# Optimization experiments

Hardware: AMD Instinct MI355X
Metric: run time of the kernel (lower is better)

Reference implementation:

```python
import jax, jax.numpy as jnp
import numpy as np

B, S, E = 16, 1024, 512
D = 2 * E            # dim of concatenated embeddings, input to QKV and MLP
H1, H2 = 2048, 1024  # hidden_dims
SCALE = float(1.0 / np.sqrt(E))  # code scales by embedding_dim**0.5 (the init arg, not D)


def setup_inputs() -> dict:
    key = jax.random.key(0)
    k = jax.random.split(key, 12)

    def lin_w(kk, fan_in, fan_out):
        return jax.random.normal(kk, (fan_in, fan_out), jnp.float32) * float(1.0 / np.sqrt(fan_in))

    return {
        "emb1": jax.random.normal(k[0], (B, S, E), jnp.float32),
        "emb2": jax.random.normal(k[1], (B, S, E), jnp.float32),
        # query-row masks; all ones (a 0 would -inf an entire softmax row -> NaN)
        "mask1": jnp.ones((B, S // 2), jnp.int32),
        "mask2": jnp.ones((B, S // 2), jnp.int32),
        "Wq": lin_w(k[2], D, D), "bq": jnp.zeros((D,), jnp.float32),
        "Wk": lin_w(k[3], D, D), "bk": jnp.zeros((D,), jnp.float32),
        "Wv": lin_w(k[4], D, D), "bv": jnp.zeros((D,), jnp.float32),
        "W1": lin_w(k[5], D, H1), "b1": jnp.zeros((H1,), jnp.float32),
        "W2": lin_w(k[6], H1, H2), "b2": jnp.zeros((H2,), jnp.float32),
        "W3": lin_w(k[7], H2, 1), "b3": jnp.zeros((1,), jnp.float32),
    }


def reference(emb1, emb2, mask1, mask2, Wq, bq, Wk, bk, Wv, bv, W1, b1, W2, b2, W3, b3):
    x = jnp.concatenate([emb1, emb2], axis=-1)        # [B, S, D]
    mask = jnp.concatenate([mask1, mask2], axis=-1)   # [B, S] (query-row mask)

    # QKV self-attention with query-only mask
    Q = x @ Wq + bq
    K = x @ Wk + bk
    V = x @ Wv + bv
    scores = jnp.einsum("bqd,bkd->bqk", Q, K) * SCALE  # [B, S, S]
    scores = jnp.where(mask[:, :, None] == 0, -jnp.inf, scores)
    attn = jax.nn.softmax(scores, axis=-1)
    attended = jnp.einsum("bqk,bkd->bqd", attn, V)     # [B, S, D]

    # MLP head (Dropout is identity in eval mode)
    h = jax.nn.relu(attended @ W1 + b1)
    h = jax.nn.relu(h @ W2 + b2)
    logits = h @ W3 + b3                               # [B, S, 1]
    return jax.nn.sigmoid(logits)
```

## Files before the change

### kernel.cpp

```cpp
#include <hip/hip_runtime.h>
#include <math.h>

#define DEV __device__ __forceinline__

typedef unsigned short u16;
typedef unsigned int   u32;
typedef __bf16 bf16x8 __attribute__((ext_vector_type(8)));
typedef float  f32x4  __attribute__((ext_vector_type(4)));
typedef u16    u16x8  __attribute__((ext_vector_type(8)));
typedef u16    u16x4  __attribute__((ext_vector_type(4)));

DEV u16 f2b(float f) {
  u32 u = __builtin_bit_cast(u32, f);
  u = (u + 0x7FFFu + ((u >> 16) & 1u)) >> 16;
  return (u16)u;
}
DEV float b2f(u16 h) { u32 u = (u32)h << 16; return __builtin_bit_cast(float, u); }

DEV void gl_lds16(const u16* g, u16* l) {
  __builtin_amdgcn_global_load_lds((const __attribute__((address_space(1))) void*)g,
                                   (__attribute__((address_space(3))) void*)l, 16, 0, 0);
}

DEV float wred_max(float v) {
#pragma unroll
  for (int o = 32; o > 0; o >>= 1) v = fmaxf(v, __shfl_xor(v, o, 64));
  return v;
}
DEV float wred_sum(float v) {
#pragma unroll
  for (int o = 32; o > 0; o >>= 1) v += __shfl_xor(v, o, 64);
  return v;
}

__global__ __launch_bounds__(256) void concat_convert(
    const float* __restrict__ e1, const float* __restrict__ e2, u16* __restrict__ xb) {
  const size_t idx = ((size_t)blockIdx.x * 256 + threadIdx.x) * 8;
  const int d = (int)(idx & 1023);
  const size_t row = idx >> 10;
  const float* s = (d < 512) ? (e1 + row * 512 + d) : (e2 + row * 512 + (d - 512));
  f32x4 a = *(const f32x4*)s;
  f32x4 b = *(const f32x4*)(s + 4);
  u16x8 o;
  o[0]=f2b(a[0]); o[1]=f2b(a[1]); o[2]=f2b(a[2]); o[3]=f2b(a[3]);
  o[4]=f2b(b[0]); o[5]=f2b(b[1]); o[6]=f2b(b[2]); o[7]=f2b(b[3]);
  *(u16x8*)(xb + idx) = o;
}

__global__ __launch_bounds__(256) void transpose_w(
    const float* __restrict__ W, int ldi, u16* __restrict__ WT, int ldo) {
  __shared__ float tile[64][65];
  const int tx = threadIdx.x & 63, ty = threadIdx.x >> 6;
  const int r0 = blockIdx.y * 64, c0 = blockIdx.x * 64;
#pragma unroll
  for (int i = 0; i < 16; ++i)
    tile[ty + 4*i][tx] = W[(size_t)(r0 + ty + 4*i) * ldi + c0 + tx];
  __syncthreads();
#pragma unroll
  for (int i = 0; i < 16; ++i)
    WT[(size_t)(c0 + ty + 4*i) * ldo + r0 + tx] = f2b(tile[tx][ty + 4*i]);
}

__global__ void concat_bias(const float* __restrict__ bq, const float* __restrict__ bk,
                            float* __restrict__ o) {
  int i = blockIdx.x * 256 + threadIdx.x;
  o[i] = (i < 1024) ? bq[i] : bk[i - 1024];
}

template<int F32OUT, int RELU, int RBIAS>
__global__ __launch_bounds__(512, 2) void gemm256(
    const u16* __restrict__ A, int lda, long long sA,
    const u16* __restrict__ B, int ldb, long long sB,
    void* __restrict__ C, int ldc, long long sC,
    const float* __restrict__ bias, float scale, int K) {
  __shared__ __align__(16) u16 lds[4][2][8192];

  const int t  = threadIdx.x;
  const int ln = t & 63, wv = t >> 6;

  int bx, by, bz;
  {
    const int gx = gridDim.x, gy = gridDim.y, gz = gridDim.z;
    const int nwg = gx * gy * gz;
    const int F = (blockIdx.z * gy + blockIdx.y) * gx + blockIdx.x;
    const int q = nwg >> 3;
    const int L = (F & 7) * q + (F >> 3);
    if (gz > 1) {
      const int pb = gx * gy;
      bz = L / pb; const int r = L - bz * pb;
      by = r / gx; bx = r - by * gx;
    } else {
      bz = 0;
      const int sh = ((gy & 7) == 0) ? 8 : 4;
      const int sw = gx * sh;
      const int sy = L / sw; const int r = L - sy * sw;
      bx = r / sh; by = sy * sh + (r - bx * sh);
    }
  }
  const int m0 = by * 256, n0 = bx * 256;
  A += (size_t)bz * (size_t)sA; B += (size_t)bz * (size_t)sB;

  const int srow = t >> 2;
  const int sgr  = (t & 3) ^ ((t >> 3) & 3);
  const u16* gA = A + (size_t)(m0 + srow) * lda + sgr * 8;
  const u16* gB = B + (size_t)(n0 + srow) * ldb + sgr * 8;
  const size_t a128 = (size_t)128 * lda, b128 = (size_t)128 * ldb;
  const int ldst = wv * 512;

  const int l15 = ln & 15, lhi = ln >> 4;
  const int wm = (wv >> 2) * 128, wn = (wv & 3) * 64;

  int offA[8], offB[4];
#pragma unroll
  for (int i = 0; i < 8; ++i) {
    const int r = wm + i * 16 + l15;
    offA[i] = r * 32 + ((lhi ^ ((r >> 1) & 3)) << 3);
  }
#pragma unroll
  for (int j = 0; j < 4; ++j) {
    const int r = wn + j * 16 + l15;
    offB[j] = r * 32 + ((lhi ^ ((r >> 1) & 3)) << 3);
  }

  f32x4 acc[8][4] = {};
  const int KT = K >> 5;

#pragma unroll
  for (int pt = 0; pt < 3; ++pt) {
    const u16* _ga = gA + (size_t)pt * 32;
    const u16* _gb = gB + (size_t)pt * 32;
    u16* _la = &lds[pt][0][ldst];
    u16* _lb = &lds[pt][1][ldst];
    gl_lds16(_ga, _la); gl_lds16(_ga + a128, _la + 4096);
    gl_lds16(_gb, _lb); gl_lds16(_gb + b128, _lb + 4096);
  }
  asm volatile("s_waitcnt vmcnt(8)" ::: "memory");
  __builtin_amdgcn_sched_barrier(0);
  __builtin_amdgcn_s_barrier();

  for (int kt = 0; kt < KT; ++kt) {
    const u16* Abuf = &lds[kt & 3][0][0];
    const u16* Bbuf = &lds[kt & 3][1][0];
    const int  nt   = kt + 3;

    if (nt < KT) {
      const u16* _ga = gA + (size_t)nt * 32;
      const u16* _gb = gB + (size_t)nt * 32;
      u16* _la = &lds[nt & 3][0][ldst];
      u16* _lb = &lds[nt & 3][1][ldst];
      gl_lds16(_ga, _la); gl_lds16(_ga + a128, _la + 4096);
      gl_lds16(_gb, _lb); gl_lds16(_gb + b128, _lb + 4096);
    }

    bf16x8 a0 = *(const bf16x8*)&Abuf[offA[0]];
    bf16x8 a1 = *(const bf16x8*)&Abuf[offA[1]];
    bf16x8 a2 = *(const bf16x8*)&Abuf[offA[2]];
    bf16x8 a3 = *(const bf16x8*)&Abuf[offA[3]];
    bf16x8 b0 = *(const bf16x8*)&Bbuf[offB[0]];
    bf16x8 b1 = *(const bf16x8*)&Bbuf[offB[1]];
    bf16x8 b2 = *(const bf16x8*)&Bbuf[offB[2]];
    bf16x8 b3 = *(const bf16x8*)&Bbuf[offB[3]];
    bf16x8 a4 = *(const bf16x8*)&Abuf[offA[4]];
    bf16x8 a5 = *(const bf16x8*)&Abuf[offA[5]];
    bf16x8 a6 = *(const bf16x8*)&Abuf[offA[6]];
    bf16x8 a7 = *(const bf16x8*)&Abuf[offA[7]];

    __builtin_amdgcn_s_setprio(1);
    acc[0][0] = __builtin_amdgcn_mfma_f32_16x16x32_bf16(a0, b0, acc[0][0], 0, 0, 0);
    acc[0][1] = __builtin_amdgcn_mfma_f32_16x16x32_bf16(a0, b1, acc[0][1], 0, 0, 0);
    acc[0][2] = __builtin_amdgcn_mfma_f32_16x16x32_bf16(a0, b2, acc[0][2], 0, 0, 0);
    acc[0][3] = __builtin_amdgcn_mfma_f32_16x16x32_bf16(a0, b3, acc[0][3], 0, 0, 0);
    acc[1][0] = __builtin_amdgcn_mfma_f32_16x16x32_bf16(a1, b0, acc[1][0], 0, 0, 0);
    acc[1][1] = __builtin_amdgcn_mfma_f32_16x16x32_bf16(a1, b1, acc[1][1], 0, 0, 0);
    acc[1][2] = __builtin_amdgcn_mfma_f32_16x16x32_bf16(a1, b2, acc[1][2], 0, 0, 0);
    acc[1][3] = __builtin_amdgcn_mfma_f32_16x16x32_bf16(a1, b3, acc[1][3], 0, 0, 0);
    acc[2][0] = __builtin_amdgcn_mfma_f32_16x16x32_bf16(a2, b0, acc[2][0], 0, 0, 0);
    acc[2][1] = __builtin_amdgcn_mfma_f32_16x16x32_bf16(a2, b1, acc[2][1], 0, 0, 0);
    acc[2][2] = __builtin_amdgcn_mfma_f32_16x16x32_bf16(a2, b2, acc[2][2], 0, 0, 0);
    acc[2][3] = __builtin_amdgcn_mfma_f32_16x16x32_bf16(a2, b3, acc[2][3], 0, 0, 0);
    acc[3][0] = __builtin_amdgcn_mfma_f32_16x16x32_bf16(a3, b0, acc[3][0], 0, 0, 0);
    acc[3][1] = __builtin_amdgcn_mfma_f32_16x16x32_bf16(a3, b1, acc[3][1], 0, 0, 0);
    acc[3][2] = __builtin_amdgcn_mfma_f32_16x16x32_bf16(a3, b2, acc[3][2], 0, 0, 0);
    acc[3][3] = __builtin_amdgcn_mfma_f32_16x16x32_bf16(a3, b3, acc[3][3], 0, 0, 0);
    acc[4][0] = __builtin_amdgcn_mfma_f32_16x16x32_bf16(a4, b0, acc[4][0], 0, 0, 0);
    acc[4][1] = __builtin_amdgcn_mfma_f32_16x16x32_bf16(a4, b1, acc[4][1], 0, 0, 0);
    acc[4][2] = __builtin_amdgcn_mfma_f32_16x16x32_bf16(a4, b2, acc[4][2], 0, 0, 0);
    acc[4][3] = __builtin_amdgcn_mfma_f32_16x16x32_bf16(a4, b3, acc[4][3], 0, 0, 0);
    acc[5][0] = __builtin_amdgcn_mfma_f32_16x16x32_bf16(a5, b0, acc[5][0], 0, 0, 0);
    acc[5][1] = __builtin_amdgcn_mfma_f32_16x16x32_bf16(a5, b1, acc[5][1], 0, 0, 0);
    acc[5][2] = __builtin_amdgcn_mfma_f32_16x16x32_bf16(a5, b2, acc[5][2], 0, 0, 0);
    acc[5][3] = __builtin_amdgcn_mfma_f32_16x16x32_bf16(a5, b3, acc[5][3], 0, 0, 0);
    acc[6][0] = __builtin_amdgcn_mfma_f32_16x16x32_bf16(a6, b0, acc[6][0], 0, 0, 0);
    acc[6][1] = __builtin_amdgcn_mfma_f32_16x16x32_bf16(a6, b1, acc[6][1], 0, 0, 0);
    acc[6][2] = __builtin_amdgcn_mfma_f32_16x16x32_bf16(a6, b2, acc[6][2], 0, 0, 0);
    acc[6][3] = __builtin_amdgcn_mfma_f32_16x16x32_bf16(a6, b3, acc[6][3], 0, 0, 0);
    acc[7][0] = __builtin_amdgcn_mfma_f32_16x16x32_bf16(a7, b0, acc[7][0], 0, 0, 0);
    acc[7][1] = __builtin_amdgcn_mfma_f32_16x16x32_bf16(a7, b1, acc[7][1], 0, 0, 0);
    acc[7][2] = __builtin_amdgcn_mfma_f32_16x16x32_bf16(a7, b2, acc[7][2], 0, 0, 0);
    acc[7][3] = __builtin_amdgcn_mfma_f32_16x16x32_bf16(a7, b3, acc[7][3], 0, 0, 0);
    __builtin_amdgcn_s_setprio(0);

    if (kt < KT - 3)       { asm volatile("s_waitcnt vmcnt(8)" ::: "memory"); }
    else if (kt == KT - 3) { asm volatile("s_waitcnt vmcnt(4)" ::: "memory"); }
    else if (kt == KT - 2) { asm volatile("s_waitcnt vmcnt(0)" ::: "memory"); }
    __builtin_amdgcn_sched_barrier(0);
    __builtin_amdgcn_s_barrier();
  }

  const size_t cb = (size_t)bz * (size_t)sC;
#pragma unroll
  for (int i = 0; i < 8; ++i) {
    const int rg = m0 + wm + i * 16 + lhi * 4;
#pragma unroll
    for (int j = 0; j < 4; ++j) {
      const int cg = n0 + wn + j * 16 + l15;
      const float cbv = (!RBIAS && bias) ? bias[cg] : 0.f;
#pragma unroll
      for (int r = 0; r < 4; ++r) {
        float v = acc[i][j][r] * scale + (RBIAS ? bias[rg + r] : cbv);
        if (RELU) v = fmaxf(v, 0.f);
        if (F32OUT) ((float*)C)[cb + (size_t)(rg + r) * ldc + cg] = v;
        else        ((u16*)C)[cb + (size_t)(rg + r) * ldc + cg] = f2b(v);
      }
    }
  }
}

__global__ __launch_bounds__(256) void softmax_mask(
    const float* __restrict__ sc, const int* __restrict__ m1,
    const int* __restrict__ m2, u16* __restrict__ attn) {
  __shared__ float red[8];
  const int row = blockIdx.x;
  const int b = row >> 10, q = row & 1023;
  const int mk = (q < 512) ? m1[b * 512 + q] : m2[b * 512 + q - 512];
  f32x4 v = ((const f32x4*)(sc + (size_t)row * 1024))[threadIdx.x];
  if (mk == 0) { v[0] = v[1] = v[2] = v[3] = -INFINITY; }
  float mx = fmaxf(fmaxf(v[0], v[1]), fmaxf(v[2], v[3]));
  mx = wred_max(mx);
  const int ln = threadIdx.x & 63, wv = threadIdx.x >> 6;
  if (ln == 0) red[wv] = mx;
  __syncthreads();
  mx = fmaxf(fmaxf(red[0], red[1]), fmaxf(red[2], red[3]));
  float e0 = __expf(v[0] - mx), e1 = __expf(v[1] - mx);
  float e2 = __expf(v[2] - mx), e3 = __expf(v[3] - mx);
  float s = wred_sum(e0 + e1 + e2 + e3);
  if (ln == 0) red[4 + wv] = s;
  __syncthreads();
  const float inv = 1.f / (red[4] + red[5] + red[6] + red[7]);
  u16x4 o; o[0] = f2b(e0 * inv); o[1] = f2b(e1 * inv); o[2] = f2b(e2 * inv); o[3] = f2b(e3 * inv);
  *(u16x4*)(attn + (size_t)row * 1024 + threadIdx.x * 4) = o;
}

__global__ __launch_bounds__(256) void logits_sigmoid(
    const u16* __restrict__ h2, const float* __restrict__ W3,
    const float* __restrict__ b3, float* __restrict__ out) {
  const int wid = (blockIdx.x * 256 + threadIdx.x) >> 6;
  const int ln = threadIdx.x & 63;
  const u16* r = h2 + (size_t)wid * 1024 + ln * 16;
  u16x8 v0 = *(const u16x8*)r;
  u16x8 v1 = *(const u16x8*)(r + 8);
  const float* w = W3 + ln * 16;
  float s = 0.f;
#pragma unroll
  for (int i = 0; i < 8; ++i) s += b2f(v0[i]) * w[i];
#pragma unroll
  for (int i = 0; i < 8; ++i) s += b2f(v1[i]) * w[8 + i];
#pragma unroll
  for (int o = 32; o > 0; o >>= 1) s += __shfl_down(s, o, 64);
  if (ln == 0) out[wid] = 1.f / (1.f + __expf(-(s + b3[0])));
}

extern "C" void kernel_launch(void* const* d_in, const int* in_sizes, int n_in,
                              void* d_out, int out_size, void* d_ws, size_t ws_size,
                              hipStream_t stream) {
  (void)in_sizes; (void)n_in; (void)out_size; (void)ws_size;
  const float* emb1 = (const float*)d_in[0];
  const float* emb2 = (const float*)d_in[1];
  const int*   mask1 = (const int*)d_in[2];
  const int*   mask2 = (const int*)d_in[3];
  const float* Wq = (const float*)d_in[4];  const float* bq = (const float*)d_in[5];
  const float* Wk = (const float*)d_in[6];  const float* bk = (const float*)d_in[7];
  const float* Wv = (const float*)d_in[8];  const float* bv = (const float*)d_in[9];
  const float* W1 = (const float*)d_in[10]; const float* b1 = (const float*)d_in[11];
  const float* W2 = (const float*)d_in[12]; const float* b2 = (const float*)d_in[13];
  const float* W3 = (const float*)d_in[14]; const float* b3 = (const float*)d_in[15];

  char* ws = (char*)d_ws;
  u16*  XB    = (u16*)(ws + 0);
  u16*  QK    = (u16*)(ws + 33554432);
  u16*  VT    = (u16*)(ws + 100663296);
  float* SC   = (float*)(ws + 134217728);
  u16*  WTQKV = (u16*)(ws + 201326592);
  u16*  W1T   = (u16*)(ws + 207618048);
  u16*  W2T   = (u16*)(ws + 211812352);
  float* BF_  = (float*)(ws + 216006656);
  u16*  ATTN  = XB;
  u16*  ATT   = (u16*)(ws + 134217728);
  u16*  H1    = QK;
  u16*  H2    = VT;
  float* out  = (float*)d_out;

  const float SCALE = 0.04419417382415922f;

  concat_convert<<<8192, 256, 0, stream>>>(emb1, emb2, XB);
  transpose_w<<<dim3(16, 16), 256, 0, stream>>>(Wq, 1024, WTQKV, 1024);
  transpose_w<<<dim3(16, 16), 256, 0, stream>>>(Wk, 1024, WTQKV + 1024 * 1024, 1024);
  transpose_w<<<dim3(16, 16), 256, 0, stream>>>(Wv, 1024, WTQKV + 2048 * 1024, 1024);
  transpose_w<<<dim3(32, 16), 256, 0, stream>>>(W1, 2048, W1T, 1024);
  transpose_w<<<dim3(16, 32), 256, 0, stream>>>(W2, 1024, W2T, 2048);
  concat_bias<<<8, 256, 0, stream>>>(bq, bk, BF_);

  gemm256<0, 0, 0><<<dim3(8, 64, 1), 512, 0, stream>>>(
      XB, 1024, 0, WTQKV, 1024, 0, QK, 2048, 0, BF_, 1.f, 1024);
  gemm256<0, 0, 1><<<dim3(64, 4, 1), 512, 0, stream>>>(
      WTQKV + 2048 * 1024, 1024, 0, XB, 1024, 0, VT, 16384, 0, bv, 1.f, 1024);
  gemm256<1, 0, 0><<<dim3(4, 4, 16), 512, 0, stream>>>(
      QK, 2048, 2097152LL, QK + 1024, 2048, 2097152LL,
      SC, 1024, 1048576LL, nullptr, SCALE, 1024);
  softmax_mask<<<16384, 256, 0, stream>>>(SC, mask1, mask2, ATTN);
  gemm256<0, 0, 0><<<dim3(4, 4, 16), 512, 0, stream>>>(
      ATTN, 1024, 1048576LL, VT, 16384, 1024LL,
      ATT, 1024, 1048576LL, nullptr, 1.f, 1024);
  gemm256<0, 1, 0><<<dim3(8, 64, 1), 512, 0, stream>>>(
      ATT, 1024, 0, W1T, 1024, 0, H1, 2048, 0, b1, 1.f, 1024);
  gemm256<0, 1, 0><<<dim3(4, 64, 1), 512, 0, stream>>>(
      H1, 2048, 0, W2T, 2048, 0, H2, 1024, 0, b2, 1.f, 2048);
  logits_sigmoid<<<4096, 256, 0, stream>>>(H2, W3, b3, out);
}
```

Baseline: 404.0 us.

## Shrink GEMM tiles to 128x128 with 256 threads and triple-buffered LDS

```diff
diff --git a/kernel.cpp b/kernel.cpp
--- a/kernel.cpp
+++ b/kernel.cpp
@@ -68,12 +68,12 @@
 }
 
 template<int F32OUT, int RELU, int RBIAS>
-__global__ __launch_bounds__(512, 2) void gemm256(
+__global__ __launch_bounds__(256, 3) void gemm128(
     const u16* __restrict__ A, int lda, long long sA,
     const u16* __restrict__ B, int ldb, long long sB,
     void* __restrict__ C, int ldc, long long sC,
     const float* __restrict__ bias, float scale, int K) {
-  __shared__ __align__(16) u16 lds[4][2][8192];
+  __shared__ __align__(16) u16 sm[3 * 8192];
 
   const int t  = threadIdx.x;
   const int ln = t & 63, wv = t >> 6;
@@ -91,79 +91,69 @@
       by = r / gx; bx = r - by * gx;
     } else {
       bz = 0;
-      const int sh = ((gy & 7) == 0) ? 8 : 4;
-      const int sw = gx * sh;
+      const int sw = gx * 8;
       const int sy = L / sw; const int r = L - sy * sw;
-      bx = r / sh; by = sy * sh + (r - bx * sh);
+      bx = r >> 3; by = sy * 8 + (r & 7);
     }
   }
-  const int m0 = by * 256, n0 = bx * 256;
+  const int m0 = by * 128, n0 = bx * 128;
   A += (size_t)bz * (size_t)sA; B += (size_t)bz * (size_t)sB;
 
   const int srow = t >> 2;
   const int sgr  = (t & 3) ^ ((t >> 3) & 3);
   const u16* gA = A + (size_t)(m0 + srow) * lda + sgr * 8;
   const u16* gB = B + (size_t)(n0 + srow) * ldb + sgr * 8;
-  const size_t a128 = (size_t)128 * lda, b128 = (size_t)128 * ldb;
+  const size_t a64 = (size_t)64 * lda, b64 = (size_t)64 * ldb;
   const int ldst = wv * 512;
 
   const int l15 = ln & 15, lhi = ln >> 4;
-  const int wm = (wv >> 2) * 128, wn = (wv & 3) * 64;
-
-  int offA[8], offB[4];
-#pragma unroll
-  for (int i = 0; i < 8; ++i) {
+  const int wm = (wv >> 1) * 64, wn = (wv & 1) * 64;
+
+  int offA[4], offB[4];
+#pragma unroll
+  for (int i = 0; i < 4; ++i) {
     const int r = wm + i * 16 + l15;
     offA[i] = r * 32 + ((lhi ^ ((r >> 1) & 3)) << 3);
   }
 #pragma unroll
   for (int j = 0; j < 4; ++j) {
     const int r = wn + j * 16 + l15;
-    offB[j] = r * 32 + ((lhi ^ ((r >> 1) & 3)) << 3);
-  }
-
-  f32x4 acc[8][4] = {};
+    offB[j] = 4096 + r * 32 + ((lhi ^ ((r >> 1) & 3)) << 3);
+  }
+
+  f32x4 acc[4][4] = {};
   const int KT = K >> 5;
 
-#pragma unroll
-  for (int pt = 0; pt < 3; ++pt) {
-    const u16* _ga = gA + (size_t)pt * 32;
-    const u16* _gb = gB + (size_t)pt * 32;
-    u16* _la = &lds[pt][0][ldst];
-    u16* _lb = &lds[pt][1][ldst];
-    gl_lds16(_ga, _la); gl_lds16(_ga + a128, _la + 4096);
-    gl_lds16(_gb, _lb); gl_lds16(_gb + b128, _lb + 4096);
-  }
-  asm volatile("s_waitcnt vmcnt(8)" ::: "memory");
+#define STAGE(tile)                                                       \
+  {                                                                       \
+    const int rb = (tile) % 3;                                            \
+    const u16* _ga = gA + (size_t)(tile) * 32;                            \
+    const u16* _gb = gB + (size_t)(tile) * 32;                            \
+    u16* _la = &sm[rb * 8192 + ldst];                                     \
+    u16* _lb = &sm[rb * 8192 + 4096 + ldst];                              \
+    gl_lds16(_ga, _la); gl_lds16(_ga + a64, _la + 2048);                  \
+    gl_lds16(_gb, _lb); gl_lds16(_gb + b64, _lb + 2048);                  \
+  }
+
+  STAGE(0); STAGE(1);
+  asm volatile("s_waitcnt vmcnt(4)" ::: "memory");
   __builtin_amdgcn_sched_barrier(0);
   __builtin_amdgcn_s_barrier();
 
   for (int kt = 0; kt < KT; ++kt) {
-    const u16* Abuf = &lds[kt & 3][0][0];
-    const u16* Bbuf = &lds[kt & 3][1][0];
-    const int  nt   = kt + 3;
-
-    if (nt < KT) {
-      const u16* _ga = gA + (size_t)nt * 32;
-      const u16* _gb = gB + (size_t)nt * 32;
-      u16* _la = &lds[nt & 3][0][ldst];
-      u16* _lb = &lds[nt & 3][1][ldst];
-      gl_lds16(_ga, _la); gl_lds16(_ga + a128, _la + 4096);
-      gl_lds16(_gb, _lb); gl_lds16(_gb + b128, _lb + 4096);
-    }
-
-    bf16x8 a0 = *(const bf16x8*)&Abuf[offA[0]];
-    bf16x8 a1 = *(const bf16x8*)&Abuf[offA[1]];
-    bf16x8 a2 = *(const bf16x8*)&Abuf[offA[2]];
-    bf16x8 a3 = *(const bf16x8*)&Abuf[offA[3]];
-    bf16x8 b0 = *(const bf16x8*)&Bbuf[offB[0]];
-    bf16x8 b1 = *(const bf16x8*)&Bbuf[offB[1]];
-    bf16x8 b2 = *(const bf16x8*)&Bbuf[offB[2]];
-    bf16x8 b3 = *(const bf16x8*)&Bbuf[offB[3]];
-    bf16x8 a4 = *(const bf16x8*)&Abuf[offA[4]];
-    bf16x8 a5 = *(const bf16x8*)&Abuf[offA[5]];
-    bf16x8 a6 = *(const bf16x8*)&Abuf[offA[6]];
-    bf16x8 a7 = *(const bf16x8*)&Abuf[offA[7]];
+    const int rb = kt % 3;
+    const u16* Ab = &sm[rb * 8192];
+
+    if (kt + 2 < KT) STAGE(kt + 2);
+
+    bf16x8 a0 = *(const bf16x8*)&Ab[offA[0]];
+    bf16x8 a1 = *(const bf16x8*)&Ab[offA[1]];
+    bf16x8 a2 = *(const bf16x8*)&Ab[offA[2]];
+    bf16x8 a3 = *(const bf16x8*)&Ab[offA[3]];
+    bf16x8 b0 = *(const bf16x8*)&Ab[offB[0]];
+    bf16x8 b1 = *(const bf16x8*)&Ab[offB[1]];
+    bf16x8 b2 = *(const bf16x8*)&Ab[offB[2]];
+    bf16x8 b3 = *(const bf16x8*)&Ab[offB[3]];
 
     __builtin_amdgcn_s_setprio(1);
     acc[0][0] = __builtin_amdgcn_mfma_f32_16x16x32_bf16(a0, b0, acc[0][0], 0, 0, 0);
@@ -182,34 +172,20 @@
     acc[3][1] = __builtin_amdgcn_mfma_f32_16x16x32_bf16(a3, b1, acc[3][1], 0, 0, 0);
     acc[3][2] = __builtin_amdgcn_mfma_f32_16x16x32_bf16(a3, b2, acc[3][2], 0, 0, 0);
     acc[3][3] = __builtin_amdgcn_mfma_f32_16x16x32_bf16(a3, b3, acc[3][3], 0, 0, 0);
-    acc[4][0] = __builtin_amdgcn_mfma_f32_16x16x32_bf16(a4, b0, acc[4][0], 0, 0, 0);
-    acc[4][1] = __builtin_amdgcn_mfma_f32_16x16x32_bf16(a4, b1, acc[4][1], 0, 0, 0);
-    acc[4][2] = __builtin_amdgcn_mfma_f32_16x16x32_bf16(a4, b2, acc[4][2], 0, 0, 0);
-    acc[4][3] = __builtin_amdgcn_mfma_f32_16x16x32_bf16(a4, b3, acc[4][3], 0, 0, 0);
-    acc[5][0] = __builtin_amdgcn_mfma_f32_16x16x32_bf16(a5, b0, acc[5][0], 0, 0, 0);
-    acc[5][1] = __builtin_amdgcn_mfma_f32_16x16x32_bf16(a5, b1, acc[5][1], 0, 0, 0);
-    acc[5][2] = __builtin_amdgcn_mfma_f32_16x16x32_bf16(a5, b2, acc[5][2], 0, 0, 0);
-    acc[5][3] = __builtin_amdgcn_mfma_f32_16x16x32_bf16(a5, b3, acc[5][3], 0, 0, 0);
-    acc[6][0] = __builtin_amdgcn_mfma_f32_16x16x32_bf16(a6, b0, acc[6][0], 0, 0, 0);
-    acc[6][1] = __builtin_amdgcn_mfma_f32_16x16x32_bf16(a6, b1, acc[6][1], 0, 0, 0);
-    acc[6][2] = __builtin_amdgcn_mfma_f32_16x16x32_bf16(a6, b2, acc[6][2], 0, 0, 0);
-    acc[6][3] = __builtin_amdgcn_mfma_f32_16x16x32_bf16(a6, b3, acc[6][3], 0, 0, 0);
-    acc[7][0] = __builtin_amdgcn_mfma_f32_16x16x32_bf16(a7, b0, acc[7][0], 0, 0, 0);
-    acc[7][1] = __builtin_amdgcn_mfma_f32_16x16x32_bf16(a7, b1, acc[7][1], 0, 0, 0);
-    acc[7][2] = __builtin_amdgcn_mfma_f32_16x16x32_bf16(a7, b2, acc[7][2], 0, 0, 0);
-    acc[7][3] = __builtin_amdgcn_mfma_f32_16x16x32_bf16(a7, b3, acc[7][3], 0, 0, 0);
     __builtin_amdgcn_s_setprio(0);
 
-    if (kt < KT - 3)       { asm volatile("s_waitcnt vmcnt(8)" ::: "memory"); }
-    else if (kt == KT - 3) { asm volatile("s_waitcnt vmcnt(4)" ::: "memory"); }
+    if (kt < KT - 2)       { asm volatile("s_waitcnt vmcnt(4)" ::: "memory"); }
     else if (kt == KT - 2) { asm volatile("s_waitcnt vmcnt(0)" ::: "memory"); }
-    __builtin_amdgcn_sched_barrier(0);
-    __builtin_amdgcn_s_barrier();
-  }
+    if (kt < KT - 1) {
+      __builtin_amdgcn_sched_barrier(0);
+      __builtin_amdgcn_s_barrier();
+    }
+  }
+#undef STAGE
 
   const size_t cb = (size_t)bz * (size_t)sC;
 #pragma unroll
-  for (int i = 0; i < 8; ++i) {
+  for (int i = 0; i < 4; ++i) {
     const int rg = m0 + wm + i * 16 + lhi * 4;
 #pragma unroll
     for (int j = 0; j < 4; ++j) {
@@ -310,20 +286,20 @@
   transpose_w<<<dim3(16, 32), 256, 0, stream>>>(W2, 1024, W2T, 2048);
   concat_bias<<<8, 256, 0, stream>>>(bq, bk, BF_);
 
-  gemm256<0, 0, 0><<<dim3(8, 64, 1), 512, 0, stream>>>(
+  gemm128<0, 0, 0><<<dim3(16, 128, 1), 256, 0, stream>>>(
       XB, 1024, 0, WTQKV, 1024, 0, QK, 2048, 0, BF_, 1.f, 1024);
-  gemm256<0, 0, 1><<<dim3(64, 4, 1), 512, 0, stream>>>(
+  gemm128<0, 0, 1><<<dim3(128, 8, 1), 256, 0, stream>>>(
       WTQKV + 2048 * 1024, 1024, 0, XB, 1024, 0, VT, 16384, 0, bv, 1.f, 1024);
-  gemm256<1, 0, 0><<<dim3(4, 4, 16), 512, 0, stream>>>(
+  gemm128<1, 0, 0><<<dim3(8, 8, 16), 256, 0, stream>>>(
       QK, 2048, 2097152LL, QK + 1024, 2048, 2097152LL,
       SC, 1024, 1048576LL, nullptr, SCALE, 1024);
   softmax_mask<<<16384, 256, 0, stream>>>(SC, mask1, mask2, ATTN);
-  gemm256<0, 0, 0><<<dim3(4, 4, 16), 512, 0, stream>>>(
+  gemm128<0, 0, 0><<<dim3(8, 8, 16), 256, 0, stream>>>(
       ATTN, 1024, 1048576LL, VT, 16384, 1024LL,
       ATT, 1024, 1048576LL, nullptr, 1.f, 1024);
-  gemm256<0, 1, 0><<<dim3(8, 64, 1), 512, 0, stream>>>(
+  gemm128<0, 1, 0><<<dim3(16, 128, 1), 256, 0, stream>>>(
       ATT, 1024, 0, W1T, 1024, 0, H1, 2048, 0, b1, 1.f, 1024);
-  gemm256<0, 1, 0><<<dim3(4, 64, 1), 512, 0, stream>>>(
+  gemm128<0, 1, 0><<<dim3(8, 128, 1), 256, 0, stream>>>(
       H1, 2048, 0, W2T, 2048, 0, H2, 1024, 0, b2, 1.f, 2048);
   logits_sigmoid<<<4096, 256, 0, stream>>>(H2, W3, b3, out);
 }
```

New measurement: 452.5 us. 12.0% more time.

## Restructure GEMM main loop into BK=64 double-buffered ping-pong with interleaved stages

Applied to the files above, without the earlier changes.

```diff
diff --git a/kernel.cpp b/kernel.cpp
--- a/kernel.cpp
+++ b/kernel.cpp
@@ -2,6 +2,7 @@
 #include <math.h>
 
 #define DEV __device__ __forceinline__
+#define SB0() __builtin_amdgcn_sched_barrier(0)
 
 typedef unsigned short u16;
 typedef unsigned int   u32;
@@ -73,7 +74,7 @@
     const u16* __restrict__ B, int ldb, long long sB,
     void* __restrict__ C, int ldc, long long sC,
     const float* __restrict__ bias, float scale, int K) {
-  __shared__ __align__(16) u16 lds[4][2][8192];
+  __shared__ __align__(16) u16 lds[2][2][16384];
 
   const int t  = threadIdx.x;
   const int ln = t & 63, wv = t >> 6;
@@ -100,112 +101,91 @@
   const int m0 = by * 256, n0 = bx * 256;
   A += (size_t)bz * (size_t)sA; B += (size_t)bz * (size_t)sB;
 
-  const int srow = t >> 2;
-  const int sgr  = (t & 3) ^ ((t >> 3) & 3);
-  const u16* gA = A + (size_t)(m0 + srow) * lda + sgr * 8;
-  const u16* gB = B + (size_t)(n0 + srow) * ldb + sgr * 8;
-  const size_t a128 = (size_t)128 * lda, b128 = (size_t)128 * ldb;
-  const int ldst = wv * 512;
+  const int gl = (ln & 7) ^ (ln >> 3);
+  const u16* gAs = A + (size_t)(m0 + (t >> 3)) * lda + gl * 8;
+  const u16* gBs = B + (size_t)(n0 + (t >> 3)) * ldb + gl * 8;
 
   const int l15 = ln & 15, lhi = ln >> 4;
   const int wm = (wv >> 2) * 128, wn = (wv & 3) * 64;
-
-  int offA[8], offB[4];
-#pragma unroll
-  for (int i = 0; i < 8; ++i) {
-    const int r = wm + i * 16 + l15;
-    offA[i] = r * 32 + ((lhi ^ ((r >> 1) & 3)) << 3);
+  const int colk0 = ((lhi ^ (l15 & 7)) << 3);
+  const int colk1 = (((4 + lhi) ^ (l15 & 7)) << 3);
+  const int rcA = (wv >> 2) * 8192 + l15 * 64;
+  const int rcB = ((wv & 3) >> 1) * 8192 + (wv & 1) * 4096 + l15 * 64;
+
+  f32x4 acc[8][4] = {};
+  bf16x8 Af[4][2], Bf[4][2];
+  const int KT = K >> 6, NIT = KT >> 1;
+
+#define STG(T, OP, H, LD, GS)                                              \
+  if ((T) < KT) {                                                          \
+    const u16* _s = (GS) + (size_t)(H) * 128 * (size_t)(LD) + (size_t)(T) * 64; \
+    u16* _d = &lds[(T) & 1][OP][(H) * 8192 + wv * 512];                    \
+    gl_lds16(_s, _d); gl_lds16(_s + 64 * (size_t)(LD), _d + 4096);         \
   }
-#pragma unroll
-  for (int j = 0; j < 4; ++j) {
-    const int r = wn + j * 16 + l15;
-    offB[j] = r * 32 + ((lhi ^ ((r >> 1) & 3)) << 3);
+#define RDA(BUF, ILO) {                                                    \
+  _Pragma("unroll") for (int ii = 0; ii < 4; ++ii) {                       \
+    Af[ii][0] = *(const bf16x8*)&lds[BUF][0][rcA + ((ILO) + ii) * 1024 + colk0]; \
+    Af[ii][1] = *(const bf16x8*)&lds[BUF][0][rcA + ((ILO) + ii) * 1024 + colk1]; } }
+#define RDB(BUF, JLO) {                                                    \
+  _Pragma("unroll") for (int jj = 0; jj < 2; ++jj) {                       \
+    Bf[(JLO) + jj][0] = *(const bf16x8*)&lds[BUF][1][rcB + ((JLO) + jj) * 1024 + colk0]; \
+    Bf[(JLO) + jj][1] = *(const bf16x8*)&lds[BUF][1][rcB + ((JLO) + jj) * 1024 + colk1]; } }
+#define MM(ILO, JLO) {                                                     \
+  _Pragma("unroll") for (int ii = 0; ii < 4; ++ii)                         \
+  _Pragma("unroll") for (int jj = 0; jj < 2; ++jj) {                       \
+    acc[(ILO)+ii][(JLO)+jj] = __builtin_amdgcn_mfma_f32_16x16x32_bf16(Af[ii][0], Bf[(JLO)+jj][0], acc[(ILO)+ii][(JLO)+jj], 0, 0, 0); \
+    acc[(ILO)+ii][(JLO)+jj] = __builtin_amdgcn_mfma_f32_16x16x32_bf16(Af[ii][1], Bf[(JLO)+jj][1], acc[(ILO)+ii][(JLO)+jj], 0, 0, 0); } }
+#define BAR() __builtin_amdgcn_s_barrier()
+#define LGKM0() { asm volatile("s_waitcnt lgkmcnt(0)" ::: "memory"); SB0(); }
+#define PRIO(x) __builtin_amdgcn_s_setprio(x)
+
+  STG(0, 0, 0, lda, gAs); STG(0, 0, 1, lda, gAs);
+  STG(0, 1, 0, ldb, gBs); STG(0, 1, 1, ldb, gBs);
+  STG(1, 1, 0, ldb, gBs); STG(1, 1, 1, ldb, gBs);
+  asm volatile("s_waitcnt vmcnt(4)" ::: "memory");
+  SB0(); BAR();
+
+  for (int it = 0; it < NIT; ++it) {
+    const int T0 = it << 1, T1 = T0 + 1;
+    RDA(0, 0); RDB(0, 0); STG(T1, 0, 0, lda, gAs);
+    asm volatile("s_waitcnt lgkmcnt(8)" ::: "memory"); SB0();
+    BAR(); LGKM0();
+    PRIO(1); MM(0, 0); PRIO(0); BAR();
+    RDB(0, 2); STG(T1, 0, 1, lda, gAs); SB0();
+    BAR(); LGKM0();
+    PRIO(1); MM(0, 2); PRIO(0); BAR();
+    RDA(0, 4); STG(T0 + 2, 1, 0, ldb, gBs); SB0();
+    BAR(); LGKM0();
+    PRIO(1); MM(4, 0); PRIO(0); BAR();
+    STG(T0 + 2, 1, 1, ldb, gBs); SB0();
+    BAR();
+    PRIO(1); MM(4, 2); PRIO(0);
+    if (T0 + 2 < KT) { asm volatile("s_waitcnt vmcnt(4)" ::: "memory"); }
+    else             { asm volatile("s_waitcnt vmcnt(0)" ::: "memory"); }
+    SB0(); BAR();
+    RDA(1, 0); RDB(1, 0); STG(T0 + 2, 0, 0, lda, gAs);
+    asm volatile("s_waitcnt lgkmcnt(8)" ::: "memory"); SB0();
+    BAR(); LGKM0();
+    PRIO(1); MM(0, 0); PRIO(0); BAR();
+    RDB(1, 2); STG(T0 + 2, 0, 1, lda, gAs); SB0();
+    BAR(); LGKM0();
+    PRIO(1); MM(0, 2); PRIO(0); BAR();
+    RDA(1, 4); STG(T0 + 3, 1, 0, ldb, gBs); SB0();
+    BAR(); LGKM0();
+    PRIO(1); MM(4, 0); PRIO(0); BAR();
+    STG(T0 + 3, 1, 1, ldb, gBs); SB0();
+    BAR();
+    PRIO(1); MM(4, 2); PRIO(0);
+    if (T0 + 3 < KT) { asm volatile("s_waitcnt vmcnt(4)" ::: "memory"); }
+    SB0(); BAR();
   }
-
-  f32x4 acc[8][4] = {};
-  const int KT = K >> 5;
-
-#pragma unroll
-  for (int pt = 0; pt < 3; ++pt) {
-    const u16* _ga = gA + (size_t)pt * 32;
-    const u16* _gb = gB + (size_t)pt * 32;
-    u16* _la = &lds[pt][0][ldst];
-    u16* _lb = &lds[pt][1][ldst];
-    gl_lds16(_ga, _la); gl_lds16(_ga + a128, _la + 4096);
-    gl_lds16(_gb, _lb); gl_lds16(_gb + b128, _lb + 4096);
-  }
-  asm volatile("s_waitcnt vmcnt(8)" ::: "memory");
-  __builtin_amdgcn_sched_barrier(0);
-  __builtin_amdgcn_s_barrier();
-
-  for (int kt = 0; kt < KT; ++kt) {
-    const u16* Abuf = &lds[kt & 3][0][0];
-    const u16* Bbuf = &lds[kt & 3][1][0];
-    const int  nt   = kt + 3;
-
-    if (nt < KT) {
-      const u16* _ga = gA + (size_t)nt * 32;
-      const u16* _gb = gB + (size_t)nt * 32;
-      u16* _la = &lds[nt & 3][0][ldst];
-      u16* _lb = &lds[nt & 3][1][ldst];
-      gl_lds16(_ga, _la); gl_lds16(_ga + a128, _la + 4096);
-      gl_lds16(_gb, _lb); gl_lds16(_gb + b128, _lb + 4096);
-    }
-
-    bf16x8 a0 = *(const bf16x8*)&Abuf[offA[0]];
-    bf16x8 a1 = *(const bf16x8*)&Abuf[offA[1]];
-    bf16x8 a2 = *(const bf16x8*)&Abuf[offA[2]];
-    bf16x8 a3 = *(const bf16x8*)&Abuf[offA[3]];
-    bf16x8 b0 = *(const bf16x8*)&Bbuf[offB[0]];
-    bf16x8 b1 = *(const bf16x8*)&Bbuf[offB[1]];
-    bf16x8 b2 = *(const bf16x8*)&Bbuf[offB[2]];
-    bf16x8 b3 = *(const bf16x8*)&Bbuf[offB[3]];
-    bf16x8 a4 = *(const bf16x8*)&Abuf[offA[4]];
-    bf16x8 a5 = *(const bf16x8*)&Abuf[offA[5]];
-    bf16x8 a6 = *(const bf16x8*)&Abuf[offA[6]];
-    bf16x8 a7 = *(const bf16x8*)&Abuf[offA[7]];
-
-    __builtin_amdgcn_s_setprio(1);
-    acc[0][0] = __builtin_amdgcn_mfma_f32_16x16x32_bf16(a0, b0, acc[0][0], 0, 0, 0);
-    acc[0][1] = __builtin_amdgcn_mfma_f32_16x16x32_bf16(a0, b1, acc[0][1], 0, 0, 0);
-    acc[0][2] = __builtin_amdgcn_mfma_f32_16x16x32_bf16(a0, b2, acc[0][2], 0, 0, 0);
-    acc[0][3] = __builtin_amdgcn_mfma_f32_16x16x32_bf16(a0, b3, acc[0][3], 0, 0, 0);
-    acc[1][0] = __builtin_amdgcn_mfma_f32_16x16x32_bf16(a1, b0, acc[1][0], 0, 0, 0);
-    acc[1][1] = __builtin_amdgcn_mfma_f32_16x16x32_bf16(a1, b1, acc[1][1], 0, 0, 0);
-    acc[1][2] = __builtin_amdgcn_mfma_f32_16x16x32_bf16(a1, b2, acc[1][2], 0, 0, 0);
-    acc[1][3] = __builtin_amdgcn_mfma_f32_16x16x32_bf16(a1, b3, acc[1][3], 0, 0, 0);
-    acc[2][0] = __builtin_amdgcn_mfma_f32_16x16x32_bf16(a2, b0, acc[2][0], 0, 0, 0);
-    acc[2][1] = __builtin_amdgcn_mfma_f32_16x16x32_bf16(a2, b1, acc[2][1], 0, 0, 0);
-    acc[2][2] = __builtin_amdgcn_mfma_f32_16x16x32_bf16(a2, b2, acc[2][2], 0, 0, 0);
-    acc[2][3] = __builtin_amdgcn_mfma_f32_16x16x32_bf16(a2, b3, acc[2][3], 0, 0, 0);
-    acc[3][0] = __builtin_amdgcn_mfma_f32_16x16x32_bf16(a3, b0, acc[3][0], 0, 0, 0);
-    acc[3][1] = __builtin_amdgcn_mfma_f32_16x16x32_bf16(a3, b1, acc[3][1], 0, 0, 0);
-    acc[3][2] = __builtin_amdgcn_mfma_f32_16x16x32_bf16(a3, b2, acc[3][2], 0, 0, 0);
-    acc[3][3] = __builtin_amdgcn_mfma_f32_16x16x32_bf16(a3, b3, acc[3][3], 0, 0, 0);
-    acc[4][0] = __builtin_amdgcn_mfma_f32_16x16x32_bf16(a4, b0, acc[4][0], 0, 0, 0);
-    acc[4][1] = __builtin_amdgcn_mfma_f32_16x16x32_bf16(a4, b1, acc[4][1], 0, 0, 0);
-    acc[4][2] = __builtin_amdgcn_mfma_f32_16x16x32_bf16(a4, b2, acc[4][2], 0, 0, 0);
-    acc[4][3] = __builtin_amdgcn_mfma_f32_16x16x32_bf16(a4, b3, acc[4][3], 0, 0, 0);
-    acc[5][0] = __builtin_amdgcn_mfma_f32_16x16x32_bf16(a5, b0, acc[5][0], 0, 0, 0);
-    acc[5][1] = __builtin_amdgcn_mfma_f32_16x16x32_bf16(a5, b1, acc[5][1], 0, 0, 0);
-    acc[5][2] = __builtin_amdgcn_mfma_f32_16x16x32_bf16(a5, b2, acc[5][2], 0, 0, 0);
-    acc[5][3] = __builtin_amdgcn_mfma_f32_16x16x32_bf16(a5, b3, acc[5][3], 0, 0, 0);
-    acc[6][0] = __builtin_amdgcn_mfma_f32_16x16x32_bf16(a6, b0, acc[6][0], 0, 0, 0);
-    acc[6][1] = __builtin_amdgcn_mfma_f32_16x16x32_bf16(a6, b1, acc[6][1], 0, 0, 0);
-    acc[6][2] = __builtin_amdgcn_mfma_f32_16x16x32_bf16(a6, b2, acc[6][2], 0, 0, 0);
-    acc[6][3] = __builtin_amdgcn_mfma_f32_16x16x32_bf16(a6, b3, acc[6][3], 0, 0, 0);
-    acc[7][0] = __builtin_amdgcn_mfma_f32_16x16x32_bf16(a7, b0, acc[7][0], 0, 0, 0);
-    acc[7][1] = __builtin_amdgcn_mfma_f32_16x16x32_bf16(a7, b1, acc[7][1], 0, 0, 0);
-    acc[7][2] = __builtin_amdgcn_mfma_f32_16x16x32_bf16(a7, b2, acc[7][2], 0, 0, 0);
-    acc[7][3] = __builtin_amdgcn_mfma_f32_16x16x32_bf16(a7, b3, acc[7][3], 0, 0, 0);
-    __builtin_amdgcn_s_setprio(0);
-
-    if (kt < KT - 3)       { asm volatile("s_waitcnt vmcnt(8)" ::: "memory"); }
-    else if (kt == KT - 3) { asm volatile("s_waitcnt vmcnt(4)" ::: "memory"); }
-    else if (kt == KT - 2) { asm volatile("s_waitcnt vmcnt(0)" ::: "memory"); }
-    __builtin_amdgcn_sched_barrier(0);
-    __builtin_amdgcn_s_barrier();
-  }
+#undef STG
+#undef RDA
+#undef RDB
+#undef MM
+#undef BAR
+#undef LGKM0
+#undef PRIO
 
   const size_t cb = (size_t)bz * (size_t)sC;
 #pragma unroll
```

After: 390.7 us. -3.3%, faster.
